# Kernel tuning notes

Hardware: AMD Instinct MI355X
Metric: run time of the kernel (lower is better)

Reference implementation:

```python
import jax, jax.numpy as jnp
import numpy as np
from jax import lax

SCALE = 2
K_UP = 5


def conv2d(x, w, pad):
    return lax.conv_general_dilated(
        x, w, window_strides=(1, 1), padding=[(pad, pad), (pad, pad)],
        dimension_numbers=("NCHW", "OIHW", "NCHW"))


def bn(x, gamma, beta, mean, var, eps=1e-5):
    # eval-mode batchnorm, per-channel (NCHW)
    inv = gamma / jnp.sqrt(var + eps)
    return x * inv[None, :, None, None] + (beta - mean * inv)[None, :, None, None]


def pixel_shuffle(x, r):
    b, crr, h, w = x.shape
    c = crr // (r * r)
    x = x.reshape(b, c, r, r, h, w)
    x = x.transpose(0, 1, 4, 2, 5, 3)  # b, c, h, r, w, r
    return x.reshape(b, c, h * r, w * r)


def setup_inputs():
    key = jax.random.key(0)
    k0, k1, k2 = jax.random.split(key, 3)
    b, c, h, w = 2, 256, 64, 64
    cmid, cenc = 64, (SCALE * K_UP) ** 2  # 64, 100
    return {
        "X": jax.random.normal(k0, (b, c, h, w), jnp.float32),
        "comp_w": jax.random.normal(k1, (cmid, c, 1, 1), jnp.float32) * 0.05,
        "comp_gamma": jnp.ones((cmid,), jnp.float32),
        "comp_beta": jnp.zeros((cmid,), jnp.float32),
        "comp_mean": jnp.zeros((cmid,), jnp.float32),
        "comp_var": jnp.ones((cmid,), jnp.float32),
        "enc_w": jax.random.normal(k2, (cenc, cmid, 3, 3), jnp.float32) * 0.05,
        "enc_gamma": jnp.ones((cenc,), jnp.float32),
        "enc_beta": jnp.zeros((cenc,), jnp.float32),
        "enc_mean": jnp.zeros((cenc,), jnp.float32),
        "enc_var": jnp.ones((cenc,), jnp.float32),
        "power_p": jnp.ones((1,), jnp.float32),
    }


def reference(X, comp_w, comp_gamma, comp_beta, comp_mean, comp_var,
              enc_w, enc_gamma, enc_beta, enc_mean, enc_var, power_p):
    b, c, h, w = X.shape
    h_, w_ = h * SCALE, w * SCALE

    # kernel prediction branch
    W = conv2d(X, comp_w, 0)
    W = jax.nn.relu(bn(W, comp_gamma, comp_beta, comp_mean, comp_var))
    W = conv2d(W, enc_w, 1)
    W = bn(W, enc_gamma, enc_beta, enc_mean, enc_var)  # no relu
    W = pixel_shuffle(W, SCALE)  # (b, k_up^2, h_, w_)

    # power-normalized softmax: W = softmax(clamp(W)^clamp(p)) over taps
    i = jnp.clip(power_p, 1e-5)  # PowerIndex -> learnable scalar exponent
    W = jnp.clip(W, 1e-5)
    W = jnp.power(W, i[0])
    W = jax.nn.softmax(W, axis=1)

    # content branch: nearest upsample then dilated unfold (k=5, dil=2, pad=4)
    Xu = jnp.repeat(jnp.repeat(X, SCALE, axis=2), SCALE, axis=3)  # (b,c,h_,w_)
    pad = (K_UP // 2) * SCALE  # 4
    Xp = jnp.pad(Xu, ((0, 0), (0, 0), (pad, pad), (pad, pad)))
    patches = jnp.stack(
        [Xp[:, :, ki * SCALE: ki * SCALE + h_, kj * SCALE: kj * SCALE + w_]
         for ki in range(K_UP) for kj in range(K_UP)], axis=2)  # (b,c,25,h_,w_)

    return jnp.einsum("bkhw,bckhw->bchw", W, patches)
```

## Files before the change

kernel.cpp:

```cpp
#include <hip/hip_runtime.h>
#include <math.h>

#define NPX 4096
#define H2 128
#define W2 128
#define PP 66

__global__ __launch_bounds__(256) void k1_conv1x1(
    const float* __restrict__ X, const float* __restrict__ w,
    const float* __restrict__ g, const float* __restrict__ bt,
    const float* __restrict__ m, const float* __restrict__ var,
    float* __restrict__ mid_p)
{
    __shared__ float red[3 * 4 * 64];
    int tid = threadIdx.x;
    int x = tid & 63;
    int ciq = __builtin_amdgcn_readfirstlane(tid >> 6);
    int bx = blockIdx.x;
    int bb = bx >> 6, y = bx & 63;
    int co0 = blockIdx.y * 4;
    int ci0 = ciq * 64;

    const float* xp = X + ((size_t)(bb * 256 + ci0)) * NPX + y * 64 + x;
    const float* wp = w + (size_t)co0 * 256 + ci0;

    float acc[4] = {0.f, 0.f, 0.f, 0.f};

    #pragma unroll 8
    for (int ci = 0; ci < 64; ++ci) {
        float xv = xp[(size_t)ci * NPX];
        #pragma unroll
        for (int j = 0; j < 4; ++j)
            acc[j] += xv * wp[j * 256 + ci];
    }

    if (ciq > 0) {
        #pragma unroll
        for (int j = 0; j < 4; ++j)
            red[((ciq - 1) * 4 + j) * 64 + x] = acc[j];
    }
    __syncthreads();
    if (ciq == 0) {
        #pragma unroll
        for (int j = 0; j < 4; ++j) {
            float a = acc[j] + red[(0 * 4 + j) * 64 + x]
                             + red[(1 * 4 + j) * 64 + x]
                             + red[(2 * 4 + j) * 64 + x];
            int co = co0 + j;
            float inv = g[co] * rsqrtf(var[co] + 1e-5f);
            a = fmaxf(a * inv + (bt[co] - m[co] * inv), 0.f);
            mid_p[((size_t)(bb * 64 + co) * PP + (y + 1)) * PP + (x + 1)] = a;
        }
    }
}

__global__ __launch_bounds__(256) void k2a_conv3x3(
    const float* __restrict__ mid_p, const float* __restrict__ ew,
    float* __restrict__ enc)
{
    __shared__ float red[3 * 10 * 64];
    int tid = threadIdx.x;
    int x = tid & 63;
    int ciq = __builtin_amdgcn_readfirstlane(tid >> 6);
    int bx = blockIdx.x;
    int bb = bx >> 6, y = bx & 63;
    int co0 = blockIdx.y * 10;

    float acc[10];
    #pragma unroll
    for (int j = 0; j < 10; ++j) acc[j] = 0.f;

    const float* wb = ew + ((size_t)co0 * 64 + ciq * 16) * 9;

    #pragma unroll 2
    for (int ci = 0; ci < 16; ++ci) {
        const float* P = mid_p + (((size_t)(bb * 64 + ciq * 16 + ci)) * PP + y) * PP + x;
        float v0 = P[0],       v1 = P[1],          v2 = P[2];
        float v3 = P[PP],      v4 = P[PP + 1],     v5 = P[PP + 2];
        float v6 = P[2 * PP],  v7 = P[2 * PP + 1], v8 = P[2 * PP + 2];
        const float* wp = wb + ci * 9;
        #pragma unroll
        for (int j = 0; j < 10; ++j) {
            const float* wj = wp + j * 576;
            acc[j] += v0 * wj[0] + v1 * wj[1] + v2 * wj[2]
                    + v3 * wj[3] + v4 * wj[4] + v5 * wj[5]
                    + v6 * wj[6] + v7 * wj[7] + v8 * wj[8];
        }
    }

    if (ciq > 0) {
        #pragma unroll
        for (int j = 0; j < 10; ++j)
            red[((ciq - 1) * 10 + j) * 64 + x] = acc[j];
    }
    __syncthreads();
    if (ciq == 0) {
        #pragma unroll
        for (int j = 0; j < 10; ++j) {
            float a = acc[j] + red[(0 * 10 + j) * 64 + x]
                             + red[(1 * 10 + j) * 64 + x]
                             + red[(2 * 10 + j) * 64 + x];
            enc[((size_t)bb * 100 + co0 + j) * NPX + y * 64 + x] = a;
        }
    }
}

__global__ __launch_bounds__(64) void k2b_softmax(
    const float* __restrict__ enc,
    const float* __restrict__ g, const float* __restrict__ bt,
    const float* __restrict__ m, const float* __restrict__ var,
    const float* __restrict__ power_p,
    float* __restrict__ wn)
{
    int s = blockIdx.x & 3;
    int p = (blockIdx.x >> 2) * 64 + threadIdx.x;
    int bb = p >> 12, sp = p & (NPX - 1);
    float pw = fmaxf(power_p[0], 1e-5f);
    float tv[25];
    float mx = -1e30f;
    #pragma unroll
    for (int k = 0; k < 25; ++k) {
        int co = 4 * k + s;
        float inv = g[co] * rsqrtf(var[co] + 1e-5f);
        float e = enc[((size_t)bb * 100 + co) * NPX + sp] * inv + (bt[co] - m[co] * inv);
        e = fmaxf(e, 1e-5f);
        float xq = exp2f(pw * log2f(e));
        tv[k] = xq;
        mx = fmaxf(mx, xq);
    }
    float sum = 0.f;
    #pragma unroll
    for (int k = 0; k < 25; ++k) {
        float e = expf(tv[k] - mx);
        tv[k] = e;
        sum += e;
    }
    float r = 1.0f / sum;
    #pragma unroll
    for (int k = 0; k < 25; ++k)
        wn[((size_t)bb * 100 + s * 25 + k) * NPX + sp] = tv[k] * r;
}

__global__ __launch_bounds__(256) void k3_carafe(
    const float* __restrict__ X, const float* __restrict__ wn,
    float* __restrict__ out)
{
    __shared__ float xt[16 * 5 * 72];
    int tid = threadIdx.x;
    int px = tid & 63;
    int s = __builtin_amdgcn_readfirstlane(tid >> 6);
    int dy = s >> 1, dx = s & 1;
    int bx = blockIdx.x;
    int bb = bx >> 6, y = bx & 63;
    int c0 = blockIdx.y * 16;

    float wv[25];
    const float* wsrc = wn + ((size_t)bb * 100 + s * 25) * NPX + y * 64 + px;
    #pragma unroll
    for (int k = 0; k < 25; ++k)
        wv[k] = wsrc[(size_t)k * NPX];

    for (int idx = tid; idx < 5760; idx += 256) {
        int ch = idx / 360;
        int rem = idx - ch * 360;
        int r = rem / 72, c = rem - r * 72;
        int gy = y + r - 2, gx = c - 2;
        float val = 0.f;
        if (c < 68 && (unsigned)gy < 64u && (unsigned)gx < 64u)
            val = X[((size_t)(bb * 256 + c0 + ch)) * NPX + gy * 64 + gx];
        xt[idx] = val;
    }
    __syncthreads();

    int y2 = 2 * y + dy, x2 = 2 * px + dx;
    float* ob = out + ((size_t)(bb * 256 + c0) * H2 + y2) * W2 + x2;
    for (int ch = 0; ch < 16; ++ch) {
        const float* xb = &xt[ch * 360 + px];
        float a = 0.f;
        #pragma unroll
        for (int ki = 0; ki < 5; ++ki)
            #pragma unroll
            for (int kj = 0; kj < 5; ++kj)
                a += wv[ki * 5 + kj] * xb[ki * 72 + kj];
        ob[(size_t)ch * H2 * W2] = a;
    }
}

extern "C" void kernel_launch(void* const* d_in, const int* in_sizes, int n_in,
                              void* d_out, int out_size, void* d_ws, size_t ws_size,
                              hipStream_t stream)
{
    const float* X  = (const float*)d_in[0];
    const float* cw = (const float*)d_in[1];
    const float* cg = (const float*)d_in[2];
    const float* cb = (const float*)d_in[3];
    const float* cm = (const float*)d_in[4];
    const float* cv = (const float*)d_in[5];
    const float* ew = (const float*)d_in[6];
    const float* eg = (const float*)d_in[7];
    const float* eb = (const float*)d_in[8];
    const float* em = (const float*)d_in[9];
    const float* ev = (const float*)d_in[10];
    const float* pp = (const float*)d_in[11];
    float* out = (float*)d_out;

    float* ws   = (float*)d_ws;
    float* midp = ws;
    float* enc  = ws + 557568;
    float* wn   = ws + 557568 + 819200;

    hipMemsetAsync(midp, 0, 557568 * sizeof(float), stream);
    k1_conv1x1<<<dim3(128, 16), 256, 0, stream>>>(X, cw, cg, cb, cm, cv, midp);
    k2a_conv3x3<<<dim3(128, 10), 256, 0, stream>>>(midp, ew, enc);
    k2b_softmax<<<dim3(512), 64, 0, stream>>>(enc, eg, eb, em, ev, pp, wn);
    k3_carafe<<<dim3(128, 16), 256, 0, stream>>>(X, wn, out);
}
```

Before: 157.3 us.

## Fuse 3x3 conv with softmax, pre-pad X, compute four subpixels per thread

```diff
diff --git a/kernel.cpp b/kernel.cpp
--- a/kernel.cpp
+++ b/kernel.cpp
@@ -5,12 +5,13 @@
 #define H2 128
 #define W2 128
 #define PP 66
+#define XPP 68
 
 __global__ __launch_bounds__(256) void k1_conv1x1(
     const float* __restrict__ X, const float* __restrict__ w,
     const float* __restrict__ g, const float* __restrict__ bt,
     const float* __restrict__ m, const float* __restrict__ var,
-    float* __restrict__ mid_p)
+    float* __restrict__ mid_p, float* __restrict__ Xp)
 {
     __shared__ float red[3 * 4 * 64];
     int tid = threadIdx.x;
@@ -20,15 +21,18 @@
     int bb = bx >> 6, y = bx & 63;
     int co0 = blockIdx.y * 4;
     int ci0 = ciq * 64;
+    bool dopad = (blockIdx.y == 0);
 
     const float* xp = X + ((size_t)(bb * 256 + ci0)) * NPX + y * 64 + x;
     const float* wp = w + (size_t)co0 * 256 + ci0;
+    float* xpad = Xp + ((size_t)(bb * 256 + ci0) * XPP + (y + 2)) * XPP + (x + 2);
 
     float acc[4] = {0.f, 0.f, 0.f, 0.f};
 
     #pragma unroll 8
     for (int ci = 0; ci < 64; ++ci) {
         float xv = xp[(size_t)ci * NPX];
+        if (dopad) xpad[(size_t)ci * (XPP * XPP)] = xv;
         #pragma unroll
         for (int j = 0; j < 4; ++j)
             acc[j] += xv * wp[j * 256 + ci];
@@ -54,135 +58,115 @@
     }
 }
 
-__global__ __launch_bounds__(256) void k2a_conv3x3(
+__global__ __launch_bounds__(256) void k2_fused(
     const float* __restrict__ mid_p, const float* __restrict__ ew,
-    float* __restrict__ enc)
-{
-    __shared__ float red[3 * 10 * 64];
-    int tid = threadIdx.x;
-    int x = tid & 63;
-    int ciq = __builtin_amdgcn_readfirstlane(tid >> 6);
-    int bx = blockIdx.x;
-    int bb = bx >> 6, y = bx & 63;
-    int co0 = blockIdx.y * 10;
-
-    float acc[10];
-    #pragma unroll
-    for (int j = 0; j < 10; ++j) acc[j] = 0.f;
-
-    const float* wb = ew + ((size_t)co0 * 64 + ciq * 16) * 9;
-
-    #pragma unroll 2
-    for (int ci = 0; ci < 16; ++ci) {
-        const float* P = mid_p + (((size_t)(bb * 64 + ciq * 16 + ci)) * PP + y) * PP + x;
-        float v0 = P[0],       v1 = P[1],          v2 = P[2];
-        float v3 = P[PP],      v4 = P[PP + 1],     v5 = P[PP + 2];
-        float v6 = P[2 * PP],  v7 = P[2 * PP + 1], v8 = P[2 * PP + 2];
-        const float* wp = wb + ci * 9;
-        #pragma unroll
-        for (int j = 0; j < 10; ++j) {
-            const float* wj = wp + j * 576;
-            acc[j] += v0 * wj[0] + v1 * wj[1] + v2 * wj[2]
-                    + v3 * wj[3] + v4 * wj[4] + v5 * wj[5]
-                    + v6 * wj[6] + v7 * wj[7] + v8 * wj[8];
-        }
-    }
-
-    if (ciq > 0) {
-        #pragma unroll
-        for (int j = 0; j < 10; ++j)
-            red[((ciq - 1) * 10 + j) * 64 + x] = acc[j];
-    }
-    __syncthreads();
-    if (ciq == 0) {
-        #pragma unroll
-        for (int j = 0; j < 10; ++j) {
-            float a = acc[j] + red[(0 * 10 + j) * 64 + x]
-                             + red[(1 * 10 + j) * 64 + x]
-                             + red[(2 * 10 + j) * 64 + x];
-            enc[((size_t)bb * 100 + co0 + j) * NPX + y * 64 + x] = a;
-        }
-    }
-}
-
-__global__ __launch_bounds__(64) void k2b_softmax(
-    const float* __restrict__ enc,
     const float* __restrict__ g, const float* __restrict__ bt,
     const float* __restrict__ m, const float* __restrict__ var,
     const float* __restrict__ power_p,
     float* __restrict__ wn)
 {
-    int s = blockIdx.x & 3;
-    int p = (blockIdx.x >> 2) * 64 + threadIdx.x;
-    int bb = p >> 12, sp = p & (NPX - 1);
+    int tid = threadIdx.x;
+    int x = tid & 63;
+    int s = __builtin_amdgcn_readfirstlane(tid >> 6);
+    int bx = blockIdx.x;
+    int bb = bx >> 6, y = bx & 63;
+
+    const float* wb = ew + (size_t)s * 576;
+    const float* P0 = mid_p + (((size_t)bb * 64) * PP + y) * PP + x;
+
+    float acc[25];
+    #pragma unroll
+    for (int k = 0; k < 25; ++k) acc[k] = 0.f;
+
+    float v0 = P0[0],      v1 = P0[1],          v2 = P0[2];
+    float v3 = P0[PP],     v4 = P0[PP + 1],     v5 = P0[PP + 2];
+    float v6 = P0[2 * PP], v7 = P0[2 * PP + 1], v8 = P0[2 * PP + 2];
+
+    for (int ci = 0; ci < 64; ++ci) {
+        int cn = (ci < 63) ? ci + 1 : 63;
+        const float* Pn = P0 + (size_t)cn * (PP * PP);
+        float n0 = Pn[0],      n1 = Pn[1],          n2 = Pn[2];
+        float n3 = Pn[PP],     n4 = Pn[PP + 1],     n5 = Pn[PP + 2];
+        float n6 = Pn[2 * PP], n7 = Pn[2 * PP + 1], n8 = Pn[2 * PP + 2];
+
+        const float* wp = wb + ci * 9;
+        #pragma unroll
+        for (int k = 0; k < 25; ++k) {
+            const float* wj = wp + k * 2304;
+            acc[k] += v0 * wj[0] + v1 * wj[1] + v2 * wj[2]
+                    + v3 * wj[3] + v4 * wj[4] + v5 * wj[5]
+                    + v6 * wj[6] + v7 * wj[7] + v8 * wj[8];
+        }
+        v0 = n0; v1 = n1; v2 = n2; v3 = n3; v4 = n4;
+        v5 = n5; v6 = n6; v7 = n7; v8 = n8;
+    }
+
     float pw = fmaxf(power_p[0], 1e-5f);
-    float tv[25];
     float mx = -1e30f;
     #pragma unroll
     for (int k = 0; k < 25; ++k) {
         int co = 4 * k + s;
         float inv = g[co] * rsqrtf(var[co] + 1e-5f);
-        float e = enc[((size_t)bb * 100 + co) * NPX + sp] * inv + (bt[co] - m[co] * inv);
+        float e = acc[k] * inv + (bt[co] - m[co] * inv);
         e = fmaxf(e, 1e-5f);
-        float xq = exp2f(pw * log2f(e));
-        tv[k] = xq;
-        mx = fmaxf(mx, xq);
+        float t = exp2f(pw * log2f(e));
+        acc[k] = t;
+        mx = fmaxf(mx, t);
     }
     float sum = 0.f;
     #pragma unroll
     for (int k = 0; k < 25; ++k) {
-        float e = expf(tv[k] - mx);
-        tv[k] = e;
+        float e = expf(acc[k] - mx);
+        acc[k] = e;
         sum += e;
     }
     float r = 1.0f / sum;
+    float* op = wn + ((size_t)bb * 100 + s * 25) * NPX + y * 64 + x;
     #pragma unroll
     for (int k = 0; k < 25; ++k)
-        wn[((size_t)bb * 100 + s * 25 + k) * NPX + sp] = tv[k] * r;
-}
-
-__global__ __launch_bounds__(256) void k3_carafe(
-    const float* __restrict__ X, const float* __restrict__ wn,
+        op[(size_t)k * NPX] = acc[k] * r;
+}
+
+__global__ __launch_bounds__(256, 2) void k3_carafe(
+    const float* __restrict__ Xp, const float* __restrict__ wn,
     float* __restrict__ out)
 {
-    __shared__ float xt[16 * 5 * 72];
     int tid = threadIdx.x;
+    int bx = blockIdx.x;
+    int bb = bx >> 4;
+    int rg = bx & 15;
+    int y = rg * 4 + (tid >> 6);
     int px = tid & 63;
-    int s = __builtin_amdgcn_readfirstlane(tid >> 6);
-    int dy = s >> 1, dx = s & 1;
-    int bx = blockIdx.x;
-    int bb = bx >> 6, y = bx & 63;
     int c0 = blockIdx.y * 16;
 
-    float wv[25];
-    const float* wsrc = wn + ((size_t)bb * 100 + s * 25) * NPX + y * 64 + px;
-    #pragma unroll
-    for (int k = 0; k < 25; ++k)
-        wv[k] = wsrc[(size_t)k * NPX];
-
-    for (int idx = tid; idx < 5760; idx += 256) {
-        int ch = idx / 360;
-        int rem = idx - ch * 360;
-        int r = rem / 72, c = rem - r * 72;
-        int gy = y + r - 2, gx = c - 2;
-        float val = 0.f;
-        if (c < 68 && (unsigned)gy < 64u && (unsigned)gx < 64u)
-            val = X[((size_t)(bb * 256 + c0 + ch)) * NPX + gy * 64 + gx];
-        xt[idx] = val;
-    }
-    __syncthreads();
-
-    int y2 = 2 * y + dy, x2 = 2 * px + dx;
-    float* ob = out + ((size_t)(bb * 256 + c0) * H2 + y2) * W2 + x2;
+    float wv[100];
+    const float* wsrc = wn + ((size_t)bb * 100) * NPX + y * 64 + px;
+    #pragma unroll
+    for (int j = 0; j < 100; ++j)
+        wv[j] = wsrc[(size_t)j * NPX];
+
+    const float* xb = Xp + ((size_t)(bb * 256 + c0) * XPP + y) * XPP + px;
+    float* ob = out + ((size_t)(bb * 256 + c0) * H2 + 2 * y) * W2 + 2 * px;
+
     for (int ch = 0; ch < 16; ++ch) {
-        const float* xb = &xt[ch * 360 + px];
-        float a = 0.f;
+        const float* P = xb + (size_t)ch * (XPP * XPP);
+        float xv[25];
         #pragma unroll
         for (int ki = 0; ki < 5; ++ki)
             #pragma unroll
             for (int kj = 0; kj < 5; ++kj)
-                a += wv[ki * 5 + kj] * xb[ki * 72 + kj];
-        ob[(size_t)ch * H2 * W2] = a;
+                xv[ki * 5 + kj] = P[ki * XPP + kj];
+        float a0 = 0.f, a1 = 0.f, a2 = 0.f, a3 = 0.f;
+        #pragma unroll
+        for (int k = 0; k < 25; ++k) {
+            a0 += wv[k]      * xv[k];
+            a1 += wv[25 + k] * xv[k];
+            a2 += wv[50 + k] * xv[k];
+            a3 += wv[75 + k] * xv[k];
+        }
+        float* o = ob + (size_t)ch * (H2 * W2);
+        *(float2*)o        = make_float2(a0, a1);
+        *(float2*)(o + W2) = make_float2(a2, a3);
     }
 }
 
@@ -206,12 +190,11 @@
 
     float* ws   = (float*)d_ws;
     float* midp = ws;
-    float* enc  = ws + 557568;
-    float* wn   = ws + 557568 + 819200;
-
-    hipMemsetAsync(midp, 0, 557568 * sizeof(float), stream);
-    k1_conv1x1<<<dim3(128, 16), 256, 0, stream>>>(X, cw, cg, cb, cm, cv, midp);
-    k2a_conv3x3<<<dim3(128, 10), 256, 0, stream>>>(midp, ew, enc);
-    k2b_softmax<<<dim3(512), 64, 0, stream>>>(enc, eg, eb, em, ev, pp, wn);
-    k3_carafe<<<dim3(128, 16), 256, 0, stream>>>(X, wn, out);
-}
+    float* Xp   = ws + 557568;
+    float* wn   = ws + 557568 + 2367488;
+
+    hipMemsetAsync(ws, 0, (557568 + 2367488) * sizeof(float), stream);
+    k1_conv1x1<<<dim3(128, 16), 256, 0, stream>>>(X, cw, cg, cb, cm, cv, midp, Xp);
+    k2_fused<<<dim3(128), 256, 0, stream>>>(midp, ew, eg, eb, em, ev, pp, wn);
+    k3_carafe<<<dim3(32, 16), 256, 0, stream>>>(Xp, wn, out);
+}
```

Result: slower. 282.6 us (+79.7%).
